# Kernel tuning notes

Measured on AMD Instinct MI355X. Metric: run time of the kernel, lower is better.

The kernel has to match this reference:

```python
import jax, jax.numpy as jnp
import numpy as np

B, N, DEG = 16, 64, 16          # batch, nodes, out-degree per node
IN_F, EDGE_F, OUT_F, H = 1024, 128, 512, 8
F = OUT_F // H                   # n_hidden = 64 (is_concat=True)
E = N * DEG                      # num_edges = 1024
SLOPE = 0.2                      # leaky relu negative slope


def setup_inputs() -> dict:
    key = jax.random.key(0)
    k0, k1, k2, k3, k4 = jax.random.split(key, 5)
    h = jax.random.normal(k0, (B, N, IN_F), dtype=jnp.float32)
    edge_attr = jax.random.normal(k1, (B, E, EDGE_F), dtype=jnp.float32)
    # deterministic adjacency: node i -> nodes (i+k) % N, k=0..DEG-1
    # (includes self-loop, so every softmax row has >=1 neighbor)
    adj = np.zeros((N, N), dtype=np.float32)
    for i in range(N):
        for k in range(DEG):
            adj[i, (i + k) % N] = 1.0
    adj_mat = jnp.asarray(np.broadcast_to(adj, (B, N, N)).copy())
    W_node = jax.random.normal(k2, (IN_F, H * F), dtype=jnp.float32) * 0.03
    W_edge = jax.random.normal(k3, (EDGE_F, H * F), dtype=jnp.float32) * 0.05
    w_attn = jax.random.normal(k4, (3 * F,), dtype=jnp.float32) * 0.1
    return {"h": h, "adj_mat": adj_mat, "edge_attr": edge_attr,
            "W_node": W_node, "W_edge": W_edge, "w_attn": w_attn}


def reference(h, adj_mat, edge_attr, W_node, W_edge, w_attn):
    # node / edge projections
    g = (h @ W_node).reshape(B, N, H, F)                  # [B,N,H,F]
    e_proj = (edge_attr @ W_edge).reshape(B, E, H, F)     # [B,E,H,F]
    # pad edge rows up to N*N (mirrors torch.cat with zero pad)
    e_proj = jnp.pad(e_proj, ((0, 0), (0, N * N - E), (0, 0), (0, 0)))
    # scatter edge features to flattened nonzero adjacency positions,
    # in row-major nonzero order == rank via exclusive cumsum
    idx = adj_mat.reshape(B, N * N).astype(jnp.int32)     # [B,N*N] of 0/1
    rank = jnp.cumsum(idx, axis=1) - idx                  # position among nonzeros
    ef = jnp.take_along_axis(e_proj, rank[:, :, None, None], axis=1)
    ef = ef * idx[:, :, None, None].astype(g.dtype)       # zero where no edge
    ef = ef.reshape(B, N, N, H, F)                        # [B,i,j,H,F]
    # attn(cat[g_i, g_j, edge]) == g_i.w1 + g_j.w2 + edge.w3
    w_i, w_j, w_e = w_attn[:F], w_attn[F:2 * F], w_attn[2 * F:]
    s_i = jnp.einsum('bnhf,f->bnh', g, w_i)
    s_j = jnp.einsum('bnhf,f->bnh', g, w_j)
    s_e = jnp.einsum('bijhf,f->bijh', ef, w_e)
    e = jax.nn.leaky_relu(s_i[:, :, None, :] + s_j[:, None, :, :] + s_e, SLOPE)
    e = jnp.where(adj_mat[..., None] > 0, e, -jnp.inf)    # mask non-edges
    a = jax.nn.softmax(e, axis=2)                         # softmax over j
    # dropout is identity in eval mode
    out = jnp.einsum('bijh,bjhf->bihf', a, g)             # weighted aggregation
    return out.reshape(B, N, H * F)                       # is_concat=True
```

## Files before the change

### kernel.cpp

```cpp
#include <hip/hip_runtime.h>
#include <hip/hip_bf16.h>
#include <stdint.h>

#define SLOPE 0.2f

typedef short s16x8 __attribute__((ext_vector_type(8)));
typedef float f32x4 __attribute__((ext_vector_type(4)));

__device__ __forceinline__ uint32_t pk_bf16(float lo, float hi) {
    uint32_t r;
    asm("v_cvt_pk_bf16_f32 %0, %1, %2" : "=v"(r) : "v"(lo), "v"(hi));
    return r;
}

__global__ __launch_bounds__(256)
void main_kernel(const float* __restrict__ hmat,
                 const float* __restrict__ adj,
                 const float* __restrict__ edge_attr,
                 const float* __restrict__ W_node,
                 const float* __restrict__ W_edge,
                 const float* __restrict__ w_attn,
                 float* __restrict__ g,
                 float* __restrict__ s_e,
                 float* __restrict__ s_i,
                 float* __restrict__ s_j,
                 int* __restrict__ row_start)
{
    __shared__ __align__(16) char U[20480];
    unsigned short* Bs = (unsigned short*)U;
    float* wvs = (float*)U;

    int bx = blockIdx.x, tid = threadIdx.x;

    if (bx < 128) {
        int head = bx & 7, mt = bx >> 3;
        int n0 = head * 64, m0 = mt * 64;
        int wave = tid >> 6, lane = tid & 63;
        int l15 = lane & 15, quad = lane >> 4;
        int wv16 = wave * 16;

        int kp = tid >> 4, nq = tid & 15;

        const float* aFrag  = hmat + (size_t)(m0 + wv16 + l15) * 1024 + quad * 8;
        const float* bpBase = W_node + (size_t)(2 * kp) * 512 + n0 + nq * 4;

        f32x4 acc[4];
        #pragma unroll
        for (int i = 0; i < 4; ++i) acc[i] = (f32x4){0.f, 0.f, 0.f, 0.f};

        float4 a0, a1, a2, a3;
        float4 b00, b01, b10, b11;

        b00 = *(const float4*)(bpBase);
        b01 = *(const float4*)(bpBase + 512);
        b10 = *(const float4*)(bpBase + 32 * 512);
        b11 = *(const float4*)(bpBase + 33 * 512);
        {
            const float* q0 = &b00.x; const float* q1 = &b01.x;
            const float* q2 = &b10.x; const float* q3 = &b11.x;
            #pragma unroll
            for (int u = 0; u < 4; ++u) {
                *(uint32_t*)&Bs[(0 * 64 + nq * 4 + u) * 40 + 2 * kp] = pk_bf16(q0[u], q1[u]);
                *(uint32_t*)&Bs[(1 * 64 + nq * 4 + u) * 40 + 2 * kp] = pk_bf16(q2[u], q3[u]);
            }
        }
        {
            const float* bp = bpBase + (size_t)64 * 512;
            b00 = *(const float4*)bp;
            b01 = *(const float4*)(bp + 512);
            b10 = *(const float4*)(bp + 32 * 512);
            b11 = *(const float4*)(bp + 33 * 512);
        }
        a0 = *(const float4*)(aFrag);
        a1 = *(const float4*)(aFrag + 4);
        a2 = *(const float4*)(aFrag + 32);
        a3 = *(const float4*)(aFrag + 36);
        __syncthreads();

        #define GITER(IT, BUF, NOT_LAST, HAS_PF2)                              \
        {                                                                      \
            union { s16x8 v; uint32_t w[4]; } A0, A1;                          \
            A0.w[0] = pk_bf16(a0.x, a0.y); A0.w[1] = pk_bf16(a0.z, a0.w);      \
            A0.w[2] = pk_bf16(a1.x, a1.y); A0.w[3] = pk_bf16(a1.z, a1.w);      \
            A1.w[0] = pk_bf16(a2.x, a2.y); A1.w[1] = pk_bf16(a2.z, a2.w);      \
            A1.w[2] = pk_bf16(a3.x, a3.y); A1.w[3] = pk_bf16(a3.z, a3.w);      \
            if (NOT_LAST) {                                                    \
                const float* ap = aFrag + ((IT) + 1) * 64;                     \
                a0 = *(const float4*)ap;        a1 = *(const float4*)(ap + 4); \
                a2 = *(const float4*)(ap + 32); a3 = *(const float4*)(ap + 36);\
            }                                                                  \
            {                                                                  \
                s16x8 af = A0.v;                                               \
                _Pragma("unroll")                                              \
                for (int nt = 0; nt < 4; ++nt) {                               \
                    s16x8 bf = *(const s16x8*)&Bs[(((BUF)*2 + 0) * 64 + nt * 16 + l15) * 40 + quad * 8]; \
                    acc[nt] = __builtin_amdgcn_mfma_f32_16x16x32_bf16(af, bf, acc[nt], 0, 0, 0); \
                }                                                              \
            }                                                                  \
            {                                                                  \
                s16x8 af = A1.v;                                               \
                _Pragma("unroll")                                              \
                for (int nt = 0; nt < 4; ++nt) {                               \
                    s16x8 bf = *(const s16x8*)&Bs[(((BUF)*2 + 1) * 64 + nt * 16 + l15) * 40 + quad * 8]; \
                    acc[nt] = __builtin_amdgcn_mfma_f32_16x16x32_bf16(af, bf, acc[nt], 0, 0, 0); \
                }                                                              \
            }                                                                  \
            if (NOT_LAST) {   \
                int sb = ((BUF) ^ 1) * 2;                                      \
                const float* q0 = &b00.x; const float* q1 = &b01.x;            \
                const float* q2 = &b10.x; const float* q3 = &b11.x;            \
                _Pragma("unroll")                                              \
                for (int u = 0; u < 4; ++u) {                                  \
                    *(uint32_t*)&Bs[((sb + 0) * 64 + nq * 4 + u) * 40 + 2 * kp] = pk_bf16(q0[u], q1[u]); \
                    *(uint32_t*)&Bs[((sb + 1) * 64 + nq * 4 + u) * 40 + 2 * kp] = pk_bf16(q2[u], q3[u]); \
                }                                                              \
            }                                                                  \
            if (HAS_PF2) {                            \
                const float* bp = bpBase + (size_t)(((IT) + 2) * 64) * 512;    \
                b00 = *(const float4*)bp;                                      \
                b01 = *(const float4*)(bp + 512);                              \
                b10 = *(const float4*)(bp + 32 * 512);                         \
                b11 = *(const float4*)(bp + 33 * 512);                         \
            }                                                                  \
            if (NOT_LAST) __syncthreads();                                     \
        }

        for (int ii = 0; ii < 8; ++ii) {
            int it = 2 * ii;
            GITER(it,     0, true,           it + 2 < 16);
            GITER(it + 1, 1, it + 1 < 15,    it + 3 < 16);
        }
        #undef GITER

        float wi[4], wj[4];
        #pragma unroll
        for (int nt = 0; nt < 4; ++nt) {
            wi[nt] = w_attn[nt * 16 + l15];
            wj[nt] = w_attn[64 + nt * 16 + l15];
        }
        float pi[4], pj[4];
        #pragma unroll
        for (int reg = 0; reg < 4; ++reg) { pi[reg] = 0.f; pj[reg] = 0.f; }
        #pragma unroll
        for (int nt = 0; nt < 4; ++nt) {
            #pragma unroll
            for (int reg = 0; reg < 4; ++reg) {
                int gm = m0 + wv16 + quad * 4 + reg;
                int gn = n0 + nt * 16 + l15;
                g[(size_t)gm * 512 + gn] = acc[nt][reg];
                pi[reg] += acc[nt][reg] * wi[nt];
                pj[reg] += acc[nt][reg] * wj[nt];
            }
        }
        #pragma unroll
        for (int mask = 1; mask < 16; mask <<= 1) {
            #pragma unroll
            for (int reg = 0; reg < 4; ++reg) {
                pi[reg] += __shfl_xor(pi[reg], mask);
                pj[reg] += __shfl_xor(pj[reg], mask);
            }
        }
        if (l15 == 0) {
            #pragma unroll
            for (int reg = 0; reg < 4; ++reg) {
                int r = m0 + wv16 + quad * 4 + reg;
                s_i[(size_t)r * 8 + head] = pi[reg];
                s_j[(size_t)r * 8 + head] = pj[reg];
            }
        }
    } else if (bx < 256) {
        {
            int c = tid & 127, halfT = tid >> 7;
            const float* we = w_attn + 128;
            #pragma unroll
            for (int hh = 0; hh < 4; ++hh) {
                int h = halfT * 4 + hh;
                float s = 0.f;
                const float* row = W_edge + (size_t)c * 512 + h * 64;
                #pragma unroll 8
                for (int f = 0; f < 64; ++f) s += row[f] * we[f];
                wvs[c * 8 + h] = s;
            }
        }
        __syncthreads();
        int e = (bx - 128) * 128 + (tid >> 1);
        int half = tid & 1;
        const float4* erow = (const float4*)(edge_attr + (size_t)e * 128 + half * 64);
        f32x4 accl = {0.f, 0.f, 0.f, 0.f};
        f32x4 acch = {0.f, 0.f, 0.f, 0.f};
        for (int c4 = 0; c4 < 16; ++c4) {
            float4 v = erow[c4];
            #pragma unroll
            for (int u = 0; u < 4; ++u) {
                int c = half * 64 + c4 * 4 + u;
                f32x4 w0 = *(const f32x4*)&wvs[c * 8];
                f32x4 w1 = *(const f32x4*)&wvs[c * 8 + 4];
                float x = (u == 0) ? v.x : (u == 1) ? v.y : (u == 2) ? v.z : v.w;
                accl += x * w0;
                acch += x * w1;
            }
        }
        #pragma unroll
        for (int q = 0; q < 4; ++q) {
            accl[q] += __shfl_xor(accl[q], 1);
            acch[q] += __shfl_xor(acch[q], 1);
        }
        if (half == 0) {
            *(f32x4*)(s_e + (size_t)e * 8)     = accl;
            *(f32x4*)(s_e + (size_t)e * 8 + 4) = acch;
        }
    } else {
        int b = bx - 256;
        if (tid < 64) {
            const float* row = adj + (size_t)b * 4096 + (size_t)tid * 64;
            int cnt = 0;
            #pragma unroll 8
            for (int j = 0; j < 64; ++j) cnt += (row[j] > 0.5f) ? 1 : 0;
            int inc = cnt;
            #pragma unroll
            for (int d = 1; d < 64; d <<= 1) {
                int u = __shfl_up(inc, d, 64);
                if (tid >= d) inc += u;
            }
            row_start[b * 64 + tid] = inc - cnt;
        }
    }
}

__global__ __launch_bounds__(256)
void attn_kernel(const float* __restrict__ g,
                 const float* __restrict__ adj,
                 const float* __restrict__ s_e,
                 const float* __restrict__ s_i,
                 const float* __restrict__ s_j,
                 const int*   __restrict__ row_start,
                 float* __restrict__ out)
{
    __shared__ float a_s[16][8];
    __shared__ int nbr[16];
    __shared__ int m_nb_s;

    int bi = blockIdx.x;
    int b = bi >> 6, i = bi & 63;
    int tid = threadIdx.x;

    if (tid < 16) nbr[tid] = 0;
    if (tid < 64) {
        float av = adj[(size_t)b * 4096 + (size_t)i * 64 + tid];
        unsigned long long m = __ballot(av > 0.5f);
        if (av > 0.5f) {
            int before = __popcll(m & ((1ull << tid) - 1ull));
            if (before < 16) nbr[before] = tid;
        }
        if (tid == 0) {
            int c = __popcll(m);
            m_nb_s = (c > 16) ? 16 : c;
        }
    }
    __syncthreads();

    int m_nb = m_nb_s;

    int c0 = tid * 2;
    int h = tid >> 5;
    float2 gv[16];
    #pragma unroll
    for (int k = 0; k < 16; ++k) {
        gv[k] = *(const float2*)(g + (size_t)(b * 64 + nbr[k]) * 512 + c0);
    }

    if (tid < 128) {
        int hh = tid >> 4, k = tid & 15;
        float v;
        if (k < m_nb) {
            int rs = row_start[bi];
            float se = s_e[(size_t)(b * 1024 + rs + k) * 8 + hh];
            float sj = s_j[(size_t)(b * 64 + nbr[k]) * 8 + hh];
            float si = s_i[(size_t)bi * 8 + hh];
            v = si + sj + se;
            v = (v >= 0.f) ? v : SLOPE * v;
        } else {
            v = -1e30f;
        }
        float mx = v;
        #pragma unroll
        for (int mask = 1; mask < 16; mask <<= 1)
            mx = fmaxf(mx, __shfl_xor(mx, mask));
        float e = (k < m_nb) ? __expf(v - mx) : 0.f;
        float ssum = e;
        #pragma unroll
        for (int mask = 1; mask < 16; mask <<= 1)
            ssum += __shfl_xor(ssum, mask);
        a_s[k][hh] = e / ssum;
    }
    __syncthreads();

    float o0 = 0.f, o1 = 0.f;
    #pragma unroll
    for (int k = 0; k < 16; ++k) {
        float ak = a_s[k][h];
        o0 += ak * gv[k].x;
        o1 += ak * gv[k].y;
    }
    out[(size_t)bi * 512 + c0]     = o0;
    out[(size_t)bi * 512 + c0 + 1] = o1;
}

extern "C" void kernel_launch(void* const* d_in, const int* in_sizes, int n_in,
                              void* d_out, int out_size, void* d_ws, size_t ws_size,
                              hipStream_t stream) {
    const float* h_in      = (const float*)d_in[0];
    const float* adj_mat   = (const float*)d_in[1];
    const float* edge_attr = (const float*)d_in[2];
    const float* W_node    = (const float*)d_in[3];
    const float* W_edge    = (const float*)d_in[4];
    const float* w_attn    = (const float*)d_in[5];
    float* out = (float*)d_out;

    char* ws = (char*)d_ws;
    float* g         = (float*)(ws + 0x000000);
    float* s_e       = (float*)(ws + 0x200000);
    float* s_i       = (float*)(ws + 0x280000);
    float* s_j       = (float*)(ws + 0x288000);
    int*   row_start = (int*)  (ws + 0x290000);

    main_kernel<<<272, 256, 0, stream>>>(h_in, adj_mat, edge_attr,
                                         W_node, W_edge, w_attn,
                                         g, s_e, s_i, s_j, row_start);
    attn_kernel<<<1024, 256, 0, stream>>>(g, adj_mat, s_e, s_i, s_j,
                                          row_start, out);
}
```

Before: 87.48 us.

## Process one attention row per wavefront and drop block barriers

The attention kernel now maps one (batch,node) row to each 64-lane wavefront, with four rows per block and 256 blocks instead of 1024. Neighbor discovery, softmax (two heads per lane) and aggregation all run within a single wave, so both __syncthreads are removed. Each lane handles 8 output columns with float4 loads and stores. The kernel relies on wave-level coherence of LDS writes without a barrier, which holds within one wave on AMD but is fragile.

```diff
diff --git a/kernel.cpp b/kernel.cpp
--- a/kernel.cpp
+++ b/kernel.cpp
@@ -236,74 +236,75 @@
                  const int*   __restrict__ row_start,
                  float* __restrict__ out)
 {
-    __shared__ float a_s[16][8];
-    __shared__ int nbr[16];
-    __shared__ int m_nb_s;
-
-    int bi = blockIdx.x;
+    __shared__ int   nbr_s[4][16];
+    __shared__ float a_s[4][16][8];
+
+    int tid = threadIdx.x;
+    int wave = tid >> 6, lane = tid & 63;
+    int bi = blockIdx.x * 4 + wave;
     int b = bi >> 6, i = bi & 63;
-    int tid = threadIdx.x;
-
-    if (tid < 16) nbr[tid] = 0;
-    if (tid < 64) {
-        float av = adj[(size_t)b * 4096 + (size_t)i * 64 + tid];
-        unsigned long long m = __ballot(av > 0.5f);
-        if (av > 0.5f) {
-            int before = __popcll(m & ((1ull << tid) - 1ull));
-            if (before < 16) nbr[before] = tid;
-        }
-        if (tid == 0) {
-            int c = __popcll(m);
-            m_nb_s = (c > 16) ? 16 : c;
-        }
-    }
-    __syncthreads();
-
-    int m_nb = m_nb_s;
-
-    int c0 = tid * 2;
-    int h = tid >> 5;
-    float2 gv[16];
-    #pragma unroll
-    for (int k = 0; k < 16; ++k) {
-        gv[k] = *(const float2*)(g + (size_t)(b * 64 + nbr[k]) * 512 + c0);
-    }
-
-    if (tid < 128) {
-        int hh = tid >> 4, k = tid & 15;
-        float v;
+
+    float av = adj[(size_t)b * 4096 + (size_t)i * 64 + lane];
+    unsigned long long m = __ballot(av > 0.5f);
+    int m_nb = __popcll(m); m_nb = (m_nb > 16) ? 16 : m_nb;
+    int before = __popcll(m & ((1ull << lane) - 1ull));
+
+    if (lane < 16) nbr_s[wave][lane] = 0;
+    if (av > 0.5f && before < 16) nbr_s[wave][before] = lane;
+
+    {
+        int k = lane & 15, h0 = lane >> 4;
+        int nk = nbr_s[wave][k];
+        float v0, v1;
         if (k < m_nb) {
             int rs = row_start[bi];
-            float se = s_e[(size_t)(b * 1024 + rs + k) * 8 + hh];
-            float sj = s_j[(size_t)(b * 64 + nbr[k]) * 8 + hh];
-            float si = s_i[(size_t)bi * 8 + hh];
-            v = si + sj + se;
-            v = (v >= 0.f) ? v : SLOPE * v;
+            float se0 = s_e[(size_t)(b * 1024 + rs + k) * 8 + h0];
+            float se1 = s_e[(size_t)(b * 1024 + rs + k) * 8 + h0 + 4];
+            float sj0 = s_j[(size_t)(b * 64 + nk) * 8 + h0];
+            float sj1 = s_j[(size_t)(b * 64 + nk) * 8 + h0 + 4];
+            float si0 = s_i[(size_t)bi * 8 + h0];
+            float si1 = s_i[(size_t)bi * 8 + h0 + 4];
+            v0 = si0 + sj0 + se0; v0 = (v0 >= 0.f) ? v0 : SLOPE * v0;
+            v1 = si1 + sj1 + se1; v1 = (v1 >= 0.f) ? v1 : SLOPE * v1;
         } else {
-            v = -1e30f;
-        }
-        float mx = v;
-        #pragma unroll
-        for (int mask = 1; mask < 16; mask <<= 1)
-            mx = fmaxf(mx, __shfl_xor(mx, mask));
-        float e = (k < m_nb) ? __expf(v - mx) : 0.f;
-        float ssum = e;
-        #pragma unroll
-        for (int mask = 1; mask < 16; mask <<= 1)
-            ssum += __shfl_xor(ssum, mask);
-        a_s[k][hh] = e / ssum;
+            v0 = -1e30f; v1 = -1e30f;
+        }
+        float mx0 = v0, mx1 = v1;
+        #pragma unroll
+        for (int mask = 1; mask < 16; mask <<= 1) {
+            mx0 = fmaxf(mx0, __shfl_xor(mx0, mask));
+            mx1 = fmaxf(mx1, __shfl_xor(mx1, mask));
+        }
+        float e0 = (k < m_nb) ? __expf(v0 - mx0) : 0.f;
+        float e1 = (k < m_nb) ? __expf(v1 - mx1) : 0.f;
+        float s0 = e0, s1 = e1;
+        #pragma unroll
+        for (int mask = 1; mask < 16; mask <<= 1) {
+            s0 += __shfl_xor(s0, mask);
+            s1 += __shfl_xor(s1, mask);
+        }
+        a_s[wave][k][h0]     = e0 / s0;
+        a_s[wave][k][h0 + 4] = e1 / s1;
     }
-    __syncthreads();
-
-    float o0 = 0.f, o1 = 0.f;
-    #pragma unroll
-    for (int k = 0; k < 16; ++k) {
-        float ak = a_s[k][h];
-        o0 += ak * gv[k].x;
-        o1 += ak * gv[k].y;
+
+    {
+        int c0 = lane * 8;
+        int h = lane >> 3;
+        float o0 = 0.f, o1 = 0.f, o2 = 0.f, o3 = 0.f;
+        float o4 = 0.f, o5 = 0.f, o6 = 0.f, o7 = 0.f;
+        #pragma unroll
+        for (int k = 0; k < 16; ++k) {
+            float ak = a_s[wave][k][h];
+            int nk = nbr_s[wave][k];
+            const float4* gp = (const float4*)(g + (size_t)(b * 64 + nk) * 512 + c0);
+            float4 ga = gp[0], gb = gp[1];
+            o0 += ak * ga.x; o1 += ak * ga.y; o2 += ak * ga.z; o3 += ak * ga.w;
+            o4 += ak * gb.x; o5 += ak * gb.y; o6 += ak * gb.z; o7 += ak * gb.w;
+        }
+        float4* op = (float4*)(out + (size_t)bi * 512 + c0);
+        op[0] = (float4){o0, o1, o2, o3};
+        op[1] = (float4){o4, o5, o6, o7};
     }
-    out[(size_t)bi * 512 + c0]     = o0;
-    out[(size_t)bi * 512 + c0 + 1] = o1;
 }
 
 extern "C" void kernel_launch(void* const* d_in, const int* in_sizes, int n_in,
@@ -327,6 +328,6 @@
     main_kernel<<<272, 256, 0, stream>>>(h_in, adj_mat, edge_attr,
                                          W_node, W_edge, w_attn,
                                          g, s_e, s_i, s_j, row_start);
-    attn_kernel<<<1024, 256, 0, stream>>>(g, adj_mat, s_e, s_i, s_j,
-                                          row_start, out);
+    attn_kernel<<<256, 256, 0, stream>>>(g, adj_mat, s_e, s_i, s_j,
+                                         row_start, out);
 }
```

Result: no change. 88.50 us (+1.2%).
